# Performance work log

Measured on AMD Instinct MI355X. Metric: run time of the kernel, lower is better.

The kernel has to match this reference:

```python
import jax, jax.numpy as jnp
import numpy as np

B, N = 16384, 2048
MASK_FILL = -1e8  # masked_fill value in non-decision-focused branch


def setup_inputs() -> dict:
    key = jax.random.key(0)
    ks = jax.random.split(key, 8)
    x = jax.random.normal(ks[0], (B, 2), dtype=jnp.float32)
    x_dist = jax.random.uniform(ks[1], (N, N), dtype=jnp.float32)
    x_features = jax.random.normal(ks[2], (B, 2), dtype=jnp.float32)
    x_markov = jax.random.uniform(ks[3], (B, N), dtype=jnp.float32)
    x_week = jax.random.randint(ks[4], (B,), 0, 7)
    x_mask = jax.random.randint(ks[5], (B, N), 0, 2).astype(jnp.int32)
    # Conv1d(1, N, 1) params: weight [N,1,1] -> only the per-channel scale
    # matters after torch.diagonal; bias [N].
    conv_w = jax.random.normal(ks[6], (N,), dtype=jnp.float32)
    conv_b = jax.random.normal(ks[7], (N,), dtype=jnp.float32) * 0.1
    return {"x": x, "x_dist": x_dist, "x_features": x_features,
            "x_markov": x_markov, "x_week": x_week, "x_mask": x_mask,
            "conv_w": conv_w, "conv_b": conv_b}


def reference(x, x_dist, x_features, x_markov, x_week, x_mask, conv_w, conv_b):
    # Conv1d(1,N,1)(x_markov[:,None,:]) yields out[b,i,j] = w[i]*x_markov[b,j] + b[i];
    # torch.diagonal(out, dim1=1, dim2=2)[b,i] = w[i]*x_markov[b,i] + b[i].
    # So the quadratic conv + diagonal collapses to a per-channel affine.
    x_ = conv_w[None, :] * x_markov + conv_b[None, :]          # [B, N]
    logp = jax.nn.log_softmax(x_, axis=1)                      # [B, N]
    return jnp.where(x_mask.astype(bool), MASK_FILL, logp)     # masked_fill
```

## Files before the change

### kernel.cpp

```cpp
#include <hip/hip_runtime.h>


#define BDIM 256
#define NCOLS 2048
#define WAVES_PER_BLOCK 4

__global__ __launch_bounds__(BDIM) void markov_logsoftmax_kernel(
    const float* __restrict__ x_markov,
    const int*   __restrict__ x_mask,
    const float* __restrict__ conv_w,
    const float* __restrict__ conv_b,
    float*       __restrict__ out)
{
    const int wave = threadIdx.x >> 6;
    const int lane = threadIdx.x & 63;
    const long long row = (long long)blockIdx.x * WAVES_PER_BLOCK + wave;

    const float* __restrict__ mrow = x_markov + row * NCOLS;
    const int*   __restrict__ krow = x_mask   + row * NCOLS;
    float*       __restrict__ orow = out      + row * NCOLS;

    float4 t[8];
    float vmax = -3.4e38f;
#pragma unroll
    for (int j = 0; j < 8; ++j) {
        const int idx = (j * 64 + lane) * 4;
        const float4 m = *(const float4*)(mrow + idx);
        const float4 w = *(const float4*)(conv_w + idx);
        const float4 b = *(const float4*)(conv_b + idx);
        float4 v;
        v.x = fmaf(w.x, m.x, b.x);
        v.y = fmaf(w.y, m.y, b.y);
        v.z = fmaf(w.z, m.z, b.z);
        v.w = fmaf(w.w, m.w, b.w);
        t[j] = v;
        vmax = fmaxf(vmax, fmaxf(fmaxf(v.x, v.y), fmaxf(v.z, v.w)));
    }

#pragma unroll
    for (int off = 32; off >= 1; off >>= 1)
        vmax = fmaxf(vmax, __shfl_xor(vmax, off, 64));

    float sum = 0.f;
#pragma unroll
    for (int j = 0; j < 8; ++j) {
        sum += __expf(t[j].x - vmax);
        sum += __expf(t[j].y - vmax);
        sum += __expf(t[j].z - vmax);
        sum += __expf(t[j].w - vmax);
    }
#pragma unroll
    for (int off = 32; off >= 1; off >>= 1)
        sum += __shfl_xor(sum, off, 64);

    const float c = vmax + __logf(sum);

#pragma unroll
    for (int j = 0; j < 8; ++j) {
        const int idx = (j * 64 + lane) * 4;
        const int4 msk = *(const int4*)(krow + idx);
        const float4 v = t[j];
        float4 o;
        o.x = msk.x ? -1e8f : (v.x - c);
        o.y = msk.y ? -1e8f : (v.y - c);
        o.z = msk.z ? -1e8f : (v.z - c);
        o.w = msk.w ? -1e8f : (v.w - c);
        *(float4*)(orow + idx) = o;
    }
}

extern "C" void kernel_launch(void* const* d_in, const int* in_sizes, int n_in,
                              void* d_out, int out_size, void* d_ws, size_t ws_size,
                              hipStream_t stream) {
    const float* x_markov = (const float*)d_in[3];
    const int*   x_mask   = (const int*)d_in[5];
    const float* conv_w   = (const float*)d_in[6];
    const float* conv_b   = (const float*)d_in[7];
    float* out = (float*)d_out;

    const int B = in_sizes[4];
    const int grid = B / WAVES_PER_BLOCK;

    markov_logsoftmax_kernel<<<grid, BDIM, 0, stream>>>(
        x_markov, x_mask, conv_w, conv_b, out);
}
```

Measured before the change: 326.2 us.

## Prefetch mask early, stage conv params in LDS, loop two rows per wave

```diff
diff --git a/kernel.cpp b/kernel.cpp
--- a/kernel.cpp
+++ b/kernel.cpp
@@ -3,69 +3,94 @@
 
 #define BDIM 256
 #define NCOLS 2048
-#define WAVES_PER_BLOCK 4
+#define ROWS_PER_WAVE 2
 
 __global__ __launch_bounds__(BDIM) void markov_logsoftmax_kernel(
     const float* __restrict__ x_markov,
     const int*   __restrict__ x_mask,
     const float* __restrict__ conv_w,
     const float* __restrict__ conv_b,
-    float*       __restrict__ out)
+    float*       __restrict__ out,
+    int B)
 {
+    __shared__ float s_w[NCOLS];
+    __shared__ float s_b[NCOLS];
+
+#pragma unroll
+    for (int i = threadIdx.x; i < NCOLS / 4; i += BDIM) {
+        ((float4*)s_w)[i] = ((const float4*)conv_w)[i];
+        ((float4*)s_b)[i] = ((const float4*)conv_b)[i];
+    }
+    __syncthreads();
+
     const int wave = threadIdx.x >> 6;
     const int lane = threadIdx.x & 63;
-    const long long row = (long long)blockIdx.x * WAVES_PER_BLOCK + wave;
+    const int gwave = blockIdx.x * (BDIM / 64) + wave;
+    const int nwaves = gridDim.x * (BDIM / 64);
 
-    const float* __restrict__ mrow = x_markov + row * NCOLS;
-    const int*   __restrict__ krow = x_mask   + row * NCOLS;
-    float*       __restrict__ orow = out      + row * NCOLS;
+    for (int r = gwave; r < B; r += nwaves) {
+        const float* __restrict__ mrow = x_markov + (long long)r * NCOLS;
+        const int*   __restrict__ krow = x_mask   + (long long)r * NCOLS;
+        float*       __restrict__ orow = out      + (long long)r * NCOLS;
 
-    float4 t[8];
-    float vmax = -3.4e38f;
-#pragma unroll
-    for (int j = 0; j < 8; ++j) {
-        const int idx = (j * 64 + lane) * 4;
-        const float4 m = *(const float4*)(mrow + idx);
-        const float4 w = *(const float4*)(conv_w + idx);
-        const float4 b = *(const float4*)(conv_b + idx);
-        float4 v;
-        v.x = fmaf(w.x, m.x, b.x);
-        v.y = fmaf(w.y, m.y, b.y);
-        v.z = fmaf(w.z, m.z, b.z);
-        v.w = fmaf(w.w, m.w, b.w);
-        t[j] = v;
-        vmax = fmaxf(vmax, fmaxf(fmaxf(v.x, v.y), fmaxf(v.z, v.w)));
-    }
+        float4 t[8];
+        int4   msk[8];
 
 #pragma unroll
-    for (int off = 32; off >= 1; off >>= 1)
-        vmax = fmaxf(vmax, __shfl_xor(vmax, off, 64));
+        for (int j = 0; j < 8; ++j) {
+            const int idx = (j * 64 + lane) * 4;
+            t[j] = *(const float4*)(mrow + idx);
+        }
+#pragma unroll
+        for (int j = 0; j < 8; ++j) {
+            const int idx = (j * 64 + lane) * 4;
+            msk[j] = *(const int4*)(krow + idx);
+        }
 
-    float sum = 0.f;
+        float vmax = -3.4e38f;
 #pragma unroll
-    for (int j = 0; j < 8; ++j) {
-        sum += __expf(t[j].x - vmax);
-        sum += __expf(t[j].y - vmax);
-        sum += __expf(t[j].z - vmax);
-        sum += __expf(t[j].w - vmax);
-    }
-#pragma unroll
-    for (int off = 32; off >= 1; off >>= 1)
-        sum += __shfl_xor(sum, off, 64);
-
-    const float c = vmax + __logf(sum);
+        for (int j = 0; j < 8; ++j) {
+            const int idx = (j * 64 + lane) * 4;
+            const float4 w = *(const float4*)(s_w + idx);
+            const float4 b = *(const float4*)(s_b + idx);
+            float4 v;
+            v.x = fmaf(w.x, t[j].x, b.x);
+            v.y = fmaf(w.y, t[j].y, b.y);
+            v.z = fmaf(w.z, t[j].z, b.z);
+            v.w = fmaf(w.w, t[j].w, b.w);
+            t[j] = v;
+            vmax = fmaxf(vmax, fmaxf(fmaxf(v.x, v.y), fmaxf(v.z, v.w)));
+        }
 
 #pragma unroll
-    for (int j = 0; j < 8; ++j) {
-        const int idx = (j * 64 + lane) * 4;
-        const int4 msk = *(const int4*)(krow + idx);
-        const float4 v = t[j];
-        float4 o;
-        o.x = msk.x ? -1e8f : (v.x - c);
-        o.y = msk.y ? -1e8f : (v.y - c);
-        o.z = msk.z ? -1e8f : (v.z - c);
-        o.w = msk.w ? -1e8f : (v.w - c);
-        *(float4*)(orow + idx) = o;
+        for (int off = 32; off >= 1; off >>= 1)
+            vmax = fmaxf(vmax, __shfl_xor(vmax, off, 64));
+
+        float sum = 0.f;
+#pragma unroll
+        for (int j = 0; j < 8; ++j) {
+            sum += __expf(t[j].x - vmax);
+            sum += __expf(t[j].y - vmax);
+            sum += __expf(t[j].z - vmax);
+            sum += __expf(t[j].w - vmax);
+        }
+#pragma unroll
+        for (int off = 32; off >= 1; off >>= 1)
+            sum += __shfl_xor(sum, off, 64);
+
+        const float c = vmax + __logf(sum);
+
+#pragma unroll
+        for (int j = 0; j < 8; ++j) {
+            const int idx = (j * 64 + lane) * 4;
+            const float4 v = t[j];
+            float4 o;
+            o.x = msk[j].x ? -1e8f : (v.x - c);
+            o.y = msk[j].y ? -1e8f : (v.y - c);
+            o.z = msk[j].z ? -1e8f : (v.z - c);
+            o.w = msk[j].w ? -1e8f : (v.w - c);
+            *(float4*)(orow + idx) = o;
+        }
     }
 }
 
@@ -79,8 +104,8 @@
     float* out = (float*)d_out;
 
     const int B = in_sizes[4];
-    const int grid = B / WAVES_PER_BLOCK;
+    const int grid = B / ((BDIM / 64) * ROWS_PER_WAVE);
 
     markov_logsoftmax_kernel<<<grid, BDIM, 0, stream>>>(
-        x_markov, x_mask, conv_w, conv_b, out);
+        x_markov, x_mask, conv_w, conv_b, out, B);
 }
```

After: 335.3 us. +2.8%, slower.

## Process two rows per wave with prefetch, early mask loads, nontemporal stores

Applied to the files above, without the earlier changes.

```diff
diff --git a/kernel.cpp b/kernel.cpp
--- a/kernel.cpp
+++ b/kernel.cpp
@@ -1,9 +1,11 @@
 #include <hip/hip_runtime.h>
 
 
-#define BDIM 256
+#define BDIM 512
 #define NCOLS 2048
-#define WAVES_PER_BLOCK 4
+#define ROWS_PER_WAVE 2
+
+typedef float nfloat4 __attribute__((ext_vector_type(4)));
 
 __global__ __launch_bounds__(BDIM) void markov_logsoftmax_kernel(
     const float* __restrict__ x_markov,
@@ -14,58 +16,80 @@
 {
     const int wave = threadIdx.x >> 6;
     const int lane = threadIdx.x & 63;
-    const long long row = (long long)blockIdx.x * WAVES_PER_BLOCK + wave;
+    const long long gw = (long long)blockIdx.x * (BDIM / 64) + wave;
+    const long long r0 = gw * ROWS_PER_WAVE;
 
-    const float* __restrict__ mrow = x_markov + row * NCOLS;
-    const int*   __restrict__ krow = x_mask   + row * NCOLS;
-    float*       __restrict__ orow = out      + row * NCOLS;
-
-    float4 t[8];
-    float vmax = -3.4e38f;
+    float4 a[8];
+    {
+        const float* __restrict__ mrow = x_markov + r0 * NCOLS;
 #pragma unroll
-    for (int j = 0; j < 8; ++j) {
-        const int idx = (j * 64 + lane) * 4;
-        const float4 m = *(const float4*)(mrow + idx);
-        const float4 w = *(const float4*)(conv_w + idx);
-        const float4 b = *(const float4*)(conv_b + idx);
-        float4 v;
-        v.x = fmaf(w.x, m.x, b.x);
-        v.y = fmaf(w.y, m.y, b.y);
-        v.z = fmaf(w.z, m.z, b.z);
-        v.w = fmaf(w.w, m.w, b.w);
-        t[j] = v;
-        vmax = fmaxf(vmax, fmaxf(fmaxf(v.x, v.y), fmaxf(v.z, v.w)));
+        for (int j = 0; j < 8; ++j)
+            a[j] = *(const float4*)(mrow + (j * 64 + lane) * 4);
     }
 
 #pragma unroll
-    for (int off = 32; off >= 1; off >>= 1)
-        vmax = fmaxf(vmax, __shfl_xor(vmax, off, 64));
+    for (int k = 0; k < ROWS_PER_WAVE; ++k) {
+        const long long r = r0 + k;
+        const int*   __restrict__ krow = x_mask + r * NCOLS;
+        float*       __restrict__ orow = out    + r * NCOLS;
 
-    float sum = 0.f;
+        float4 t[8];
+        float vmax = -3.4e38f;
 #pragma unroll
-    for (int j = 0; j < 8; ++j) {
-        sum += __expf(t[j].x - vmax);
-        sum += __expf(t[j].y - vmax);
-        sum += __expf(t[j].z - vmax);
-        sum += __expf(t[j].w - vmax);
-    }
+        for (int j = 0; j < 8; ++j) {
+            const int idx = (j * 64 + lane) * 4;
+            const float4 w = *(const float4*)(conv_w + idx);
+            const float4 b = *(const float4*)(conv_b + idx);
+            float4 v;
+            v.x = fmaf(w.x, a[j].x, b.x);
+            v.y = fmaf(w.y, a[j].y, b.y);
+            v.z = fmaf(w.z, a[j].z, b.z);
+            v.w = fmaf(w.w, a[j].w, b.w);
+            t[j] = v;
+            vmax = fmaxf(vmax, fmaxf(fmaxf(v.x, v.y), fmaxf(v.z, v.w)));
+        }
+
+        if (k + 1 < ROWS_PER_WAVE) {
+            const float* __restrict__ mnext = x_markov + (r + 1) * NCOLS;
 #pragma unroll
-    for (int off = 32; off >= 1; off >>= 1)
-        sum += __shfl_xor(sum, off, 64);
+            for (int j = 0; j < 8; ++j)
+                a[j] = *(const float4*)(mnext + (j * 64 + lane) * 4);
+        }
 
-    const float c = vmax + __logf(sum);
+        int4 msk[8];
+#pragma unroll
+        for (int j = 0; j < 8; ++j)
+            msk[j] = *(const int4*)(krow + (j * 64 + lane) * 4);
 
 #pragma unroll
-    for (int j = 0; j < 8; ++j) {
-        const int idx = (j * 64 + lane) * 4;
-        const int4 msk = *(const int4*)(krow + idx);
-        const float4 v = t[j];
-        float4 o;
-        o.x = msk.x ? -1e8f : (v.x - c);
-        o.y = msk.y ? -1e8f : (v.y - c);
-        o.z = msk.z ? -1e8f : (v.z - c);
-        o.w = msk.w ? -1e8f : (v.w - c);
-        *(float4*)(orow + idx) = o;
+        for (int off = 32; off >= 1; off >>= 1)
+            vmax = fmaxf(vmax, __shfl_xor(vmax, off, 64));
+
+        float sum = 0.f;
+#pragma unroll
+        for (int j = 0; j < 8; ++j) {
+            sum += __expf(t[j].x - vmax);
+            sum += __expf(t[j].y - vmax);
+            sum += __expf(t[j].z - vmax);
+            sum += __expf(t[j].w - vmax);
+        }
+#pragma unroll
+        for (int off = 32; off >= 1; off >>= 1)
+            sum += __shfl_xor(sum, off, 64);
+
+        const float c = vmax + __logf(sum);
+
+#pragma unroll
+        for (int j = 0; j < 8; ++j) {
+            const int idx = (j * 64 + lane) * 4;
+            const float4 v = t[j];
+            nfloat4 o;
+            o.x = msk[j].x ? -1e8f : (v.x - c);
+            o.y = msk[j].y ? -1e8f : (v.y - c);
+            o.z = msk[j].z ? -1e8f : (v.z - c);
+            o.w = msk[j].w ? -1e8f : (v.w - c);
+            __builtin_nontemporal_store(o, (nfloat4*)(orow + idx));
+        }
     }
 }
 
@@ -79,7 +103,7 @@
     float* out = (float*)d_out;
 
     const int B = in_sizes[4];
-    const int grid = B / WAVES_PER_BLOCK;
+    const int grid = B / ((BDIM / 64) * ROWS_PER_WAVE);
 
     markov_logsoftmax_kernel<<<grid, BDIM, 0, stream>>>(
         x_markov, x_mask, conv_w, conv_b, out);
```

New measurement: 339.3 us. +4.0%, slower.
